# Performance work log

Hardware: AMD Instinct MI355X
Metric: run time of the kernel (lower is better)

## Reference

```python
import jax, jax.numpy as jnp
import numpy as np

B = 32768   # batch of states (original forward is per-state; we vmap)
D = 3       # coord_dim

_W_SHAPES = [("w_h0",(3,32)),("w_y0",(3,32)),("w_yu0",(3,3)),("w_u0",(3,32)),
             ("w_h1",(32,32)),("w_z1",(32,32)),("w_zu1",(32,32)),("w_y1",(3,32)),
             ("w_yu1",(32,3)),("w_u1",(32,32)),("w_h2",(32,32)),("w_z2",(32,32)),
             ("w_zu2",(32,32)),("w_y2",(3,32)),("w_yu2",(32,3)),("w_u2",(32,32)),
             ("w_z_out",(32,1)),("w_zu_out",(32,32)),("w_y_out",(3,1)),
             ("w_yu_out",(32,3)),("w_u_out",(32,1))]
_B_SHAPES = [("b_y0",(3,)),("b_h0",(32,)),("b_0",(32,)),("b_h1",(32,)),("b_y1",(3,)),
             ("b_z1",(32,)),("b_1",(32,)),("b_h2",(32,)),("b_z2",(32,)),("b_y2",(3,)),
             ("b_2",(32,)),("b_z_out",(32,)),("b_y_out",(3,)),("b_out",(1,))]

def _make_params(key):
    n = len(_W_SHAPES) + len(_B_SHAPES) + 4
    ks = jax.random.split(key, n)
    p, i = {}, 0
    for name, sh in _W_SHAPES:   # torch .uniform_(-0.1, 0.1)
        p[name] = jax.random.uniform(ks[i], sh, jnp.float32, -0.1, 0.1); i += 1
    for name, sh in _B_SHAPES:   # torch.rand -> U[0,1)
        p[name] = jax.random.uniform(ks[i], sh, jnp.float32, 0.0, 1.0); i += 1
    # fc layers: normal init per _init_weights (stds / sqrt(16)=4), zero bias
    stds = [2.2/4.0, 0.58/4.0, 0.58*2.0/4.0, 4.0]
    shapes = [(32, 3), (32, 32), (32, 32), (1, 32)]
    for j in range(4):
        p[f"fc{j+1}_w"] = stds[j] * jax.random.normal(ks[i], shapes[j], jnp.float32); i += 1
        p[f"fc{j+1}_b"] = jnp.zeros((shapes[j][0],), jnp.float32)
    return p

def setup_inputs():
    key = jax.random.key(0)
    kx, kp = jax.random.split(key)
    inp = {"x": jax.random.normal(kx, (B, 2 * D), jnp.float32)}
    inp.update(_make_params(kp))
    return inp

def _forward(x, p):
    sp, relu = jax.nn.softplus, jax.nn.relu

    def lagr(state):
        q, y = state[:D], state[D:]
        u1 = sp(q @ p["w_h0"] + p["b_h0"])
        z1 = sp((y * (q @ p["w_yu0"] + p["b_y0"])) @ p["w_y0"] + q @ p["w_u0"] + p["b_0"])
        u2 = sp(u1 @ p["w_h1"] + p["b_h1"])
        z2 = sp((z1 * (u1 @ p["w_zu1"] + p["b_z1"])) @ relu(p["w_z1"])
                + (y * (u1 @ p["w_yu1"] + p["b_y1"])) @ p["w_y1"]
                + u1 @ p["w_u1"] + p["b_1"])
        u3 = sp(u2 @ p["w_h2"] + p["b_h2"])
        z3 = sp((z2 * (u2 @ p["w_zu2"] + p["b_z2"])) @ relu(p["w_z2"])
                + (y * (u2 @ p["w_yu2"] + p["b_y2"])) @ p["w_y2"]
                + u2 @ p["w_u2"] + p["b_2"])
        zout = sp((z3 * (u3 @ p["w_zu_out"] + p["b_z_out"])) @ relu(p["w_z_out"])
                  + (y * (u3 @ p["w_yu_out"] + p["b_y_out"])) @ p["w_y_out"]
                  + u3 @ p["w_u_out"] + p["b_out"])
        V = sp(q @ p["fc1_w"].T + p["fc1_b"])
        V = sp(V @ p["fc2_w"].T + p["fc2_b"])
        V = sp(V @ p["fc3_w"].T + p["fc3_b"])
        V = V @ p["fc4_w"].T + p["fc4_b"]
        return (zout - V)[0]  # scalar Lagrangian

    def step(state):
        dq = state[D:]
        H = jax.hessian(lagr)(state)        # (6,6)
        g = jax.grad(lagr)(state)[:D]       # dL/dq, matches jacobian row b[0,:3]
        M = H[D:, D:]                       # d2L/ddq ddq
        C = H[D:, :D]                       # d2L/ddq dq
        ddq = (g - dq @ C.T) @ jnp.linalg.inv(M).T
        dx = jnp.concatenate([dq, ddq])
        return state + 0.001 * dx           # Euler step, as in torch forward

    return jax.vmap(step)(x)

def reference(x, w_h0, w_y0, w_yu0, w_u0, w_h1, w_z1, w_zu1, w_y1, w_yu1, w_u1,
              w_h2, w_z2, w_zu2, w_y2, w_yu2, w_u2, w_z_out, w_zu_out, w_y_out,
              w_yu_out, w_u_out, b_y0, b_h0, b_0, b_h1, b_y1, b_z1, b_1, b_h2,
              b_z2, b_y2, b_2, b_z_out, b_y_out, b_out, fc1_w, fc1_b, fc2_w,
              fc2_b, fc3_w, fc3_b, fc4_w, fc4_b):
    p = dict(locals())
    xv = p.pop("x")
    return _forward(xv, p)
```

## Files before the change

kernel.cpp:

```cpp
#include <hip/hip_runtime.h>

#define NTH 256
#define B_TOTAL 32768

typedef float v2f __attribute__((ext_vector_type(2)));
typedef float v4f __attribute__((ext_vector_type(4)));

struct Ptrs { const float* p[44]; };

enum : int {
  I_X = 0,
  I_WH0 = 1, I_WY0 = 2, I_WYU0 = 3, I_WU0 = 4,
  I_WH1 = 5, I_WZ1 = 6, I_WZU1 = 7, I_WY1 = 8, I_WYU1 = 9, I_WU1 = 10,
  I_WH2 = 11, I_WZ2 = 12, I_WZU2 = 13, I_WY2 = 14, I_WYU2 = 15, I_WU2 = 16,
  I_WZO = 17, I_WZUO = 18, I_WYO = 19, I_WYUO = 20, I_WUO = 21,
  I_BY0 = 22, I_BH0 = 23, I_B0 = 24, I_BH1 = 25, I_BY1 = 26, I_BZ1 = 27, I_B1 = 28,
  I_BH2 = 29, I_BZ2 = 30, I_BY2 = 31, I_B2 = 32, I_BZO = 33, I_BYO = 34, I_BOUT = 35,
  I_FC1 = 36, I_FC1B = 37, I_FC2 = 38, I_FC2B = 39, I_FC3 = 40, I_FC3B = 41,
  I_FC4 = 42, I_FC4B = 43
};

struct V16 { float c[16]; };

__device__ __forceinline__ float spf(float x) {
  return fmaxf(x, 0.0f) + __logf(1.0f + __expf(-fabsf(x)));
}
__device__ __forceinline__ float sigf(float x) {
  return __fdividef(1.0f, 1.0f + __expf(-x));
}

__device__ __forceinline__ V16 spchain16(const V16& A, float y0, float y1, float y2) {
  V16 Z;
  float s = sigf(A.c[0]);
  float d = s * (1.0f - s);
  Z.c[0] = spf(A.c[0]);
#pragma unroll
  for (int a = 0; a < 3; ++a) Z.c[1 + a] = s * A.c[1 + a];
#pragma unroll
  for (int b = 0; b < 3; ++b) Z.c[4 + b] = s * A.c[4 + b];
  Z.c[7]  = s * A.c[7]  + d * A.c[1] * A.c[1];
  Z.c[8]  = s * A.c[8]  + d * A.c[1] * A.c[2];
  Z.c[9]  = s * A.c[9]  + d * A.c[1] * A.c[3];
  Z.c[10] = s * A.c[10] + d * A.c[2] * A.c[2];
  Z.c[11] = s * A.c[11] + d * A.c[2] * A.c[3];
  Z.c[12] = s * A.c[12] + d * A.c[3] * A.c[3];
  float ydq = y0 * A.c[4] + y1 * A.c[5] + y2 * A.c[6];
#pragma unroll
  for (int a = 0; a < 3; ++a) Z.c[13 + a] = s * A.c[13 + a] + d * A.c[1 + a] * ydq;
  return Z;
}

__device__ __forceinline__ void stageProd(float* row, const V16& Z, float S0, float S1,
                                          float S2, float S3, float y0, float y1, float y2) {
  float z0 = Z.c[0];
  float ysd = y0 * S1 + y1 * S2 + y2 * S3;
  v4f w0 = {z0 * S0, S0 * Z.c[1], S0 * Z.c[2], S0 * Z.c[3]};
  v4f w1 = {z0 * S1 + S0 * Z.c[4], z0 * S2 + S0 * Z.c[5], z0 * S3 + S0 * Z.c[6], S0 * Z.c[7]};
  v4f w2 = {S0 * Z.c[8], S0 * Z.c[9], S0 * Z.c[10], S0 * Z.c[11]};
  v4f w3 = {S0 * Z.c[12], S0 * Z.c[13] + Z.c[1] * ysd, S0 * Z.c[14] + Z.c[2] * ysd,
            S0 * Z.c[15] + Z.c[3] * ysd};
  *(v4f*)(row + 0) = w0;  *(v4f*)(row + 4) = w1;
  *(v4f*)(row + 8) = w2;  *(v4f*)(row + 12) = w3;
}

__device__ __forceinline__ V16 prodZS16(const V16& Z, float S0, float S1, float S2, float S3,
                                        float y0, float y1, float y2) {
  V16 P;
  const float Sq[3] = {S1, S2, S3};
  float ysd = y0 * S1 + y1 * S2 + y2 * S3;
  P.c[0] = Z.c[0] * S0;
#pragma unroll
  for (int a = 0; a < 3; ++a) P.c[1 + a] = S0 * Z.c[1 + a];
#pragma unroll
  for (int b = 0; b < 3; ++b) P.c[4 + b] = Z.c[0] * Sq[b] + S0 * Z.c[4 + b];
#pragma unroll
  for (int t = 0; t < 6; ++t) P.c[7 + t] = S0 * Z.c[7 + t];
#pragma unroll
  for (int a = 0; a < 3; ++a) P.c[13 + a] = S0 * Z.c[13 + a] + Z.c[1 + a] * ysd;
  return P;
}

__device__ __forceinline__ void mv16(const float* __restrict__ W, int j, const float* ps,
                                     v2f& m0, v2f& m1, v2f& m2, v2f& m3,
                                     v2f& m4, v2f& m5, v2f& m6, v2f& m7) {
#pragma unroll 4
  for (int i = 0; i < 32; ++i) {
    float w = fmaxf(W[i * 32 + j], 0.0f);
    const float* r = ps + i * 16;
    v4f r0 = *(const v4f*)(r + 0);
    v4f r1 = *(const v4f*)(r + 4);
    v4f r2 = *(const v4f*)(r + 8);
    v4f r3 = *(const v4f*)(r + 12);
    m0 += r0.xy * w; m1 += r0.zw * w;
    m2 += r1.xy * w; m3 += r1.zw * w;
    m4 += r2.xy * w; m5 += r2.zw * w;
    m6 += r3.xy * w; m7 += r3.zw * w;
  }
}

__device__ __forceinline__ void stageU_all(const float* __restrict__ Wh,
                                           const float* __restrict__ Wzu,
                                           const float* __restrict__ Wu,
                                           const float* __restrict__ Wyu, int j,
                                           const float* us,
                                           v2f& h0, v2f& h1, v2f& s0, v2f& s1,
                                           v2f& w0, v2f& w1,
                                           v2f& ta0, v2f& ta1, v2f& tb0, v2f& tb1,
                                           v2f& tc0, v2f& tc1) {
#pragma unroll 2
  for (int i = 0; i < 32; ++i) {
    v4f u = *(const v4f*)(us + i * 4);
    float wh = Wh[i * 32 + j], wz = Wzu[i * 32 + j], wu = Wu[i * 32 + j];
    h0 += u.xy * wh; h1 += u.zw * wh;
    s0 += u.xy * wz; s1 += u.zw * wz;
    w0 += u.xy * wu; w1 += u.zw * wu;
    float wy0 = Wyu[i * 3 + 0], wy1 = Wyu[i * 3 + 1], wy2 = Wyu[i * 3 + 2];
    ta0 += u.xy * wy0; ta1 += u.zw * wy0;
    tb0 += u.xy * wy1; tb1 += u.zw * wy1;
    tc0 += u.xy * wy2; tc1 += u.zw * wy2;
  }
}

__device__ __forceinline__ void buildA16(const float* __restrict__ Wy, int j, float y0, float y1,
                                         float y2, const float wv[4], const float ta[4],
                                         const float tb[4], const float tc[4], V16& A) {
  float wy0 = Wy[j], wy1 = Wy[32 + j], wy2 = Wy[64 + j];
  A.c[0] = wv[0] + y0 * ta[0] * wy0 + y1 * tb[0] * wy1 + y2 * tc[0] * wy2;
  A.c[1] = ta[0] * wy0; A.c[2] = tb[0] * wy1; A.c[3] = tc[0] * wy2;
#pragma unroll
  for (int b = 0; b < 3; ++b)
    A.c[4 + b] = wv[1 + b] + y0 * ta[1 + b] * wy0 + y1 * tb[1 + b] * wy1 + y2 * tc[1 + b] * wy2;
#pragma unroll
  for (int t6 = 0; t6 < 6; ++t6) A.c[7 + t6] = 0.0f;
  float yta = y0 * ta[1] + y1 * ta[2] + y2 * ta[3];
  float ytb = y0 * tb[1] + y1 * tb[2] + y2 * tb[3];
  float ytc = y0 * tc[1] + y1 * tc[2] + y2 * tc[3];
  A.c[13] = yta * wy0; A.c[14] = ytb * wy1; A.c[15] = ytc * wy2;
}

__global__ __launch_bounds__(NTH, 4) void lnn_step_kernel(Ptrs P, float* __restrict__ out) {
  __shared__ float pstage[4][2][32][16];
  __shared__ float ustage[4][2][32][4];

  const int tid = threadIdx.x;
  const int j = tid & 31;
  const int half = (tid >> 5) & 1;
  const int wv = tid >> 6;
  const int sample = blockIdx.x * 8 + (tid >> 5);

  float* prow = &pstage[wv][half][0][0];
  float* urow = &ustage[wv][half][0][0];

  const float* X = P.p[I_X] + sample * 6;
  const float q0 = X[0], q1 = X[1], q2 = X[2];
  const float y0 = X[3], y1 = X[4], y2 = X[5];

  float Vg0, Vg1, Vg2;
  {
    const float* fc1 = P.p[I_FC1];
    float f0 = fc1[j * 3], f1 = fc1[j * 3 + 1], f2 = fc1[j * 3 + 2];
    float hp = P.p[I_FC1B][j] + q0 * f0 + q1 * f1 + q2 * f2;
    float ss = sigf(hp);
    v4f V1 = {spf(hp), ss * f0, ss * f1, ss * f2};
    *(v4f*)(urow + j * 4) = V1;
    const float* fc2 = P.p[I_FC2] + j * 32;
    v2f a0 = {P.p[I_FC2B][j], 0.0f}, a1 = {0.0f, 0.0f};
#pragma unroll 2
    for (int r = 0; r < 8; ++r) {
      v4f w4 = *(const v4f*)(fc2 + r * 4);
      v4f u0 = *(const v4f*)(urow + (r * 4 + 0) * 4);
      v4f u1 = *(const v4f*)(urow + (r * 4 + 1) * 4);
      v4f u2 = *(const v4f*)(urow + (r * 4 + 2) * 4);
      v4f u3 = *(const v4f*)(urow + (r * 4 + 3) * 4);
      a0 += u0.xy * w4.x; a1 += u0.zw * w4.x;
      a0 += u1.xy * w4.y; a1 += u1.zw * w4.y;
      a0 += u2.xy * w4.z; a1 += u2.zw * w4.z;
      a0 += u3.xy * w4.w; a1 += u3.zw * w4.w;
    }
    float ss2 = sigf(a0.x);
    v4f V2 = {spf(a0.x), ss2 * a0.y, ss2 * a1.x, ss2 * a1.y};
    *(v4f*)(urow + j * 4) = V2;
    const float* fc3 = P.p[I_FC3] + j * 32;
    v2f b0 = {P.p[I_FC3B][j], 0.0f}, b1 = {0.0f, 0.0f};
#pragma unroll 2
    for (int r = 0; r < 8; ++r) {
      v4f w4 = *(const v4f*)(fc3 + r * 4);
      v4f u0 = *(const v4f*)(urow + (r * 4 + 0) * 4);
      v4f u1 = *(const v4f*)(urow + (r * 4 + 1) * 4);
      v4f u2 = *(const v4f*)(urow + (r * 4 + 2) * 4);
      v4f u3 = *(const v4f*)(urow + (r * 4 + 3) * 4);
      b0 += u0.xy * w4.x; b1 += u0.zw * w4.x;
      b0 += u1.xy * w4.y; b1 += u1.zw * w4.y;
      b0 += u2.xy * w4.z; b1 += u2.zw * w4.z;
      b0 += u3.xy * w4.w; b1 += u3.zw * w4.w;
    }
    float ss3 = sigf(b0.x);
    float f4 = P.p[I_FC4][j];
    Vg0 = ss3 * b0.y * f4; Vg1 = ss3 * b1.x * f4; Vg2 = ss3 * b1.y * f4;
  }

  const float* yu0 = P.p[I_WYU0];
  float t0v[3];
#pragma unroll
  for (int k = 0; k < 3; ++k)
    t0v[k] = q0 * yu0[k] + q1 * yu0[3 + k] + q2 * yu0[6 + k] + P.p[I_BY0][k];

  float u1c[4];
  {
    const float* wh0 = P.p[I_WH0];
    float w0 = wh0[j], w1 = wh0[32 + j], w2 = wh0[64 + j];
    float h = P.p[I_BH0][j] + q0 * w0 + q1 * w1 + q2 * w2;
    float ss = sigf(h);
    u1c[0] = spf(h); u1c[1] = ss * w0; u1c[2] = ss * w1; u1c[3] = ss * w2;
  }

  V16 z;
  {
    const float* Wy = P.p[I_WY0];
    const float* Wu = P.p[I_WU0];
    float wy0 = Wy[j], wy1 = Wy[32 + j], wy2 = Wy[64 + j];
    float wu0 = Wu[j], wu1 = Wu[32 + j], wu2 = Wu[64 + j];
    V16 A;
    A.c[0] = P.p[I_B0][j] + (y0 * t0v[0]) * wy0 + (y1 * t0v[1]) * wy1 + (y2 * t0v[2]) * wy2 +
             q0 * wu0 + q1 * wu1 + q2 * wu2;
    A.c[1] = t0v[0] * wy0; A.c[2] = t0v[1] * wy1; A.c[3] = t0v[2] * wy2;
#pragma unroll
    for (int b = 0; b < 3; ++b) {
      float acc = (b == 0 ? wu0 : (b == 1 ? wu1 : wu2));
      acc += y0 * yu0[b * 3 + 0] * wy0 + y1 * yu0[b * 3 + 1] * wy1 + y2 * yu0[b * 3 + 2] * wy2;
      A.c[4 + b] = acc;
    }
#pragma unroll
    for (int t = 0; t < 6; ++t) A.c[7 + t] = 0.0f;
    float yty0 = y0 * yu0[0] + y1 * yu0[3] + y2 * yu0[6];
    float yty1 = y0 * yu0[1] + y1 * yu0[4] + y2 * yu0[7];
    float yty2 = y0 * yu0[2] + y1 * yu0[5] + y2 * yu0[8];
    A.c[13] = yty0 * wy0; A.c[14] = yty1 * wy1; A.c[15] = yty2 * wy2;
    z = spchain16(A, y0, y1, y2);
  }

  float unext[4];
#pragma unroll 1
  for (int lvl = 0; lvl < 2; ++lvl) {
    const float* Wh  = P.p[lvl == 0 ? I_WH1 : I_WH2];
    const float* Wzu = P.p[lvl == 0 ? I_WZU1 : I_WZU2];
    const float* Wu  = P.p[lvl == 0 ? I_WU1 : I_WU2];
    const float* Wyu = P.p[lvl == 0 ? I_WYU1 : I_WYU2];
    const float* Wy  = P.p[lvl == 0 ? I_WY1 : I_WY2];
    const float* Wz  = P.p[lvl == 0 ? I_WZ1 : I_WZ2];
    const float* Bh  = P.p[lvl == 0 ? I_BH1 : I_BH2];
    const float* Bz  = P.p[lvl == 0 ? I_BZ1 : I_BZ2];
    const float* Bl  = P.p[lvl == 0 ? I_B1 : I_B2];
    const float* By  = P.p[lvl == 0 ? I_BY1 : I_BY2];

    const float* uc = (lvl == 0) ? u1c : unext;
    v4f uu = {uc[0], uc[1], uc[2], uc[3]};
    *(v4f*)(urow + j * 4) = uu;

    v2f h0 = {Bh[j], 0.0f}, h1 = {0.0f, 0.0f};
    v2f s0 = {Bz[j], 0.0f}, s1 = {0.0f, 0.0f};
    v2f w0 = {Bl[j], 0.0f}, w1 = {0.0f, 0.0f};
    v2f ta0 = {By[0], 0.0f}, ta1 = {0.0f, 0.0f};
    v2f tb0 = {By[1], 0.0f}, tb1 = {0.0f, 0.0f};
    v2f tc0 = {By[2], 0.0f}, tc1 = {0.0f, 0.0f};
    stageU_all(Wh, Wzu, Wu, Wyu, j, urow, h0, h1, s0, s1, w0, w1,
               ta0, ta1, tb0, tb1, tc0, tc1);
    {
      float ss = sigf(h0.x);
      unext[0] = spf(h0.x); unext[1] = ss * h0.y; unext[2] = ss * h1.x; unext[3] = ss * h1.y;
    }
    stageProd(prow + j * 16, z, s0.x, s0.y, s1.x, s1.y, y0, y1, y2);

    float wvv[4] = {w0.x, w0.y, w1.x, w1.y};
    float tav[4] = {ta0.x, ta0.y, ta1.x, ta1.y};
    float tbv[4] = {tb0.x, tb0.y, tb1.x, tb1.y};
    float tcv[4] = {tc0.x, tc0.y, tc1.x, tc1.y};
    V16 A2;
    buildA16(Wy, j, y0, y1, y2, wvv, tav, tbv, tcv, A2);

    v2f m0 = {A2.c[0], A2.c[1]},   m1 = {A2.c[2], A2.c[3]};
    v2f m2 = {A2.c[4], A2.c[5]},   m3 = {A2.c[6], A2.c[7]};
    v2f m4 = {A2.c[8], A2.c[9]},   m5 = {A2.c[10], A2.c[11]};
    v2f m6 = {A2.c[12], A2.c[13]}, m7 = {A2.c[14], A2.c[15]};
    mv16(Wz, j, prow, m0, m1, m2, m3, m4, m5, m6, m7);
    A2.c[0] = m0.x;  A2.c[1] = m0.y;  A2.c[2] = m1.x;  A2.c[3] = m1.y;
    A2.c[4] = m2.x;  A2.c[5] = m2.y;  A2.c[6] = m3.x;  A2.c[7] = m3.y;
    A2.c[8] = m4.x;  A2.c[9] = m4.y;  A2.c[10] = m5.x; A2.c[11] = m5.y;
    A2.c[12] = m6.x; A2.c[13] = m6.y; A2.c[14] = m7.x; A2.c[15] = m7.y;
    z = spchain16(A2, y0, y1, y2);
  }

  {
    v4f uu = {unext[0], unext[1], unext[2], unext[3]};
    *(v4f*)(urow + j * 4) = uu;
  }
  v2f s30 = {P.p[I_BZO][j], 0.0f}, s31 = {0.0f, 0.0f};
  v2f wo0 = {0.0f, 0.0f}, wo1 = {0.0f, 0.0f};
  v2f t3a0 = {P.p[I_BYO][0], 0.0f}, t3a1 = {0.0f, 0.0f};
  v2f t3b0 = {P.p[I_BYO][1], 0.0f}, t3b1 = {0.0f, 0.0f};
  v2f t3c0 = {P.p[I_BYO][2], 0.0f}, t3c1 = {0.0f, 0.0f};
  {
    const float* Wzuo = P.p[I_WZUO];
    const float* Wuo = P.p[I_WUO];
    const float* Wyuo = P.p[I_WYUO];
#pragma unroll 2
    for (int i = 0; i < 32; ++i) {
      v4f u = *(const v4f*)(urow + i * 4);
      float wz = Wzuo[i * 32 + j];
      s30 += u.xy * wz; s31 += u.zw * wz;
      float wu = Wuo[i];
      wo0 += u.xy * wu; wo1 += u.zw * wu;
      float wy0 = Wyuo[i * 3], wy1 = Wyuo[i * 3 + 1], wy2 = Wyuo[i * 3 + 2];
      t3a0 += u.xy * wy0; t3a1 += u.zw * wy0;
      t3b0 += u.xy * wy1; t3b1 += u.zw * wy1;
      t3c0 += u.xy * wy2; t3c1 += u.zw * wy2;
    }
  }
  const float woc[4] = {wo0.x, wo0.y, wo1.x, wo1.y};
  const float t3av[4] = {t3a0.x, t3a0.y, t3a1.x, t3a1.y};
  const float t3bv[4] = {t3b0.x, t3b0.y, t3b1.x, t3b1.y};
  const float t3cv[4] = {t3c0.x, t3c0.y, t3c1.x, t3c1.y};

  float red[19];
  {
    V16 p3 = prodZS16(z, s30.x, s30.y, s31.x, s31.y, y0, y1, y2);
    float wz = fmaxf(P.p[I_WZO][j], 0.0f);
#pragma unroll
    for (int k = 0; k < 16; ++k) red[k] = p3.c[k] * wz;
    red[16] = Vg0; red[17] = Vg1; red[18] = Vg2;
  }
#pragma unroll
  for (int m = 16; m >= 1; m >>= 1) {
#pragma unroll
    for (int k = 0; k < 19; ++k) red[k] += __shfl_xor(red[k], m, 32);
  }

  if (j == 0) {
    const float* Wyo = P.p[I_WYO];
    const float wyo0 = Wyo[0], wyo1 = Wyo[1], wyo2 = Wyo[2];
    float Av = red[0] + woc[0] + P.p[I_BOUT][0] + y0 * t3av[0] * wyo0 +
               y1 * t3bv[0] * wyo1 + y2 * t3cv[0] * wyo2;
    float Agy[3];
    Agy[0] = red[1] + t3av[0] * wyo0;
    Agy[1] = red[2] + t3bv[0] * wyo1;
    Agy[2] = red[3] + t3cv[0] * wyo2;
    float Agq[3];
#pragma unroll
    for (int b = 0; b < 3; ++b)
      Agq[b] = red[4 + b] + woc[1 + b] + y0 * t3av[1 + b] * wyo0 +
               y1 * t3bv[1 + b] * wyo1 + y2 * t3cv[1 + b] * wyo2;
    float ycq[3];
    ycq[0] = red[13] + (y0 * t3av[1] + y1 * t3av[2] + y2 * t3av[3]) * wyo0;
    ycq[1] = red[14] + (y0 * t3bv[1] + y1 * t3bv[2] + y2 * t3bv[3]) * wyo1;
    ycq[2] = red[15] + (y0 * t3cv[1] + y1 * t3cv[2] + y2 * t3cv[3]) * wyo2;
    float s = sigf(Av), d = s * (1.0f - s);

    double Mm[3][3];
    const int pa[6] = {0, 0, 0, 1, 1, 2}, pb[6] = {0, 1, 2, 1, 2, 2};
#pragma unroll
    for (int t = 0; t < 6; ++t) {
      double m = (double)s * (double)red[7 + t] +
                 (double)d * (double)Agy[pa[t]] * (double)Agy[pb[t]];
      Mm[pa[t]][pb[t]] = m; Mm[pb[t]][pa[t]] = m;
    }
    double yAgq = (double)y0 * (double)Agq[0] + (double)y1 * (double)Agq[1] +
                  (double)y2 * (double)Agq[2];
    double rr[3];
#pragma unroll
    for (int a = 0; a < 3; ++a) {
      double g = (double)s * (double)Agq[a] - (double)red[16 + a];
      double Cy = (double)s * (double)ycq[a] + (double)d * (double)Agy[a] * yAgq;
      rr[a] = g - Cy;
    }
    double a = Mm[0][0], b_ = Mm[0][1], c_ = Mm[0][2], dd = Mm[1][1], e = Mm[1][2], f = Mm[2][2];
    double A00 = dd * f - e * e, A01 = c_ * e - b_ * f, A02 = b_ * e - c_ * dd;
    double A11 = a * f - c_ * c_, A12 = b_ * c_ - a * e, A22 = a * dd - b_ * b_;
    double det = a * A00 + b_ * A01 + c_ * A02;
    double idet = 1.0 / det;
    double d0 = (A00 * rr[0] + A01 * rr[1] + A02 * rr[2]) * idet;
    double d1 = (A01 * rr[0] + A11 * rr[1] + A12 * rr[2]) * idet;
    double d2 = (A02 * rr[0] + A12 * rr[1] + A22 * rr[2]) * idet;

    float* O = out + (size_t)sample * 6;
    O[0] = q0 + 0.001f * y0;
    O[1] = q1 + 0.001f * y1;
    O[2] = q2 + 0.001f * y2;
    O[3] = y0 + 0.001f * (float)d0;
    O[4] = y1 + 0.001f * (float)d1;
    O[5] = y2 + 0.001f * (float)d2;
  }
}

extern "C" void kernel_launch(void* const* d_in, const int* in_sizes, int n_in,
                              void* d_out, int out_size, void* d_ws, size_t ws_size,
                              hipStream_t stream) {
  (void)in_sizes; (void)n_in; (void)d_ws; (void)ws_size; (void)out_size;
  Ptrs P;
  for (int i = 0; i < 44; ++i) P.p[i] = (const float*)d_in[i];
  float* out = (float*)d_out;
  dim3 grid(B_TOTAL / 8), block(NTH);
  hipLaunchKernelGGL(lnn_step_kernel, grid, block, 0, stream, P, out);
}
```

Before: 135.2 us.

## Replace scalar relu(Wz) matvec with FP64 MFMA over staged shared-memory tiles

The per-lane 32x16 scalar matvec against relu(W_z) in the hidden-level loop is replaced by a wave-level 32x32 by 32x16 matrix product using FP64 16x16x4 MFMA instructions over both half-wave sample tiles. Each lane stages its product row into shared memory, the wave multiplies collectively, and results go back to shared memory to be added into the tangent accumulators. The shared-memory row stride is padded from 16 to 20 floats to reduce bank conflicts. The FP64 MFMA rate and the float-double conversions may limit the gain, and the cross-lane shared-memory traffic has no explicit barrier beyond wave-level lockstep.

```diff
diff --git a/kernel.cpp b/kernel.cpp
--- a/kernel.cpp
+++ b/kernel.cpp
@@ -2,9 +2,11 @@
 
 #define NTH 256
 #define B_TOTAL 32768
+#define PSTR 20
 
 typedef float v2f __attribute__((ext_vector_type(2)));
 typedef float v4f __attribute__((ext_vector_type(4)));
+typedef double v4d __attribute__((ext_vector_type(4)));
 
 struct Ptrs { const float* p[44]; };
 
@@ -78,24 +80,6 @@
 #pragma unroll
   for (int a = 0; a < 3; ++a) P.c[13 + a] = S0 * Z.c[13 + a] + Z.c[1 + a] * ysd;
   return P;
-}
-
-__device__ __forceinline__ void mv16(const float* __restrict__ W, int j, const float* ps,
-                                     v2f& m0, v2f& m1, v2f& m2, v2f& m3,
-                                     v2f& m4, v2f& m5, v2f& m6, v2f& m7) {
-#pragma unroll 4
-  for (int i = 0; i < 32; ++i) {
-    float w = fmaxf(W[i * 32 + j], 0.0f);
-    const float* r = ps + i * 16;
-    v4f r0 = *(const v4f*)(r + 0);
-    v4f r1 = *(const v4f*)(r + 4);
-    v4f r2 = *(const v4f*)(r + 8);
-    v4f r3 = *(const v4f*)(r + 12);
-    m0 += r0.xy * w; m1 += r0.zw * w;
-    m2 += r1.xy * w; m3 += r1.zw * w;
-    m4 += r2.xy * w; m5 += r2.zw * w;
-    m6 += r3.xy * w; m7 += r3.zw * w;
-  }
 }
 
 __device__ __forceinline__ void stageU_all(const float* __restrict__ Wh,
@@ -139,7 +123,7 @@
 }
 
 __global__ __launch_bounds__(NTH, 4) void lnn_step_kernel(Ptrs P, float* __restrict__ out) {
-  __shared__ float pstage[4][2][32][16];
+  __shared__ float pstage[4][2][32][PSTR];
   __shared__ float ustage[4][2][32][4];
 
   const int tid = threadIdx.x;
@@ -150,6 +134,11 @@
 
   float* prow = &pstage[wv][half][0][0];
   float* urow = &ustage[wv][half][0][0];
+  float* pst0 = &pstage[wv][0][0][0];
+  float* pst1 = &pstage[wv][1][0][0];
+  const int l64 = tid & 63;
+  const int n16 = l64 & 15;
+  const int kq = l64 >> 4;
 
   const float* X = P.p[I_X] + sample * 6;
   const float q0 = X[0], q1 = X[1], q2 = X[2];
@@ -269,7 +258,31 @@
       float ss = sigf(h0.x);
       unext[0] = spf(h0.x); unext[1] = ss * h0.y; unext[2] = ss * h1.x; unext[3] = ss * h1.y;
     }
-    stageProd(prow + j * 16, z, s0.x, s0.y, s1.x, s1.y, y0, y1, y2);
+    stageProd(prow + j * PSTR, z, s0.x, s0.y, s1.x, s1.y, y0, y1, y2);
+
+    v4d a00 = {0.0, 0.0, 0.0, 0.0};
+    v4d a01 = {0.0, 0.0, 0.0, 0.0};
+    v4d a10 = {0.0, 0.0, 0.0, 0.0};
+    v4d a11 = {0.0, 0.0, 0.0, 0.0};
+#pragma unroll
+    for (int c = 0; c < 8; ++c) {
+      const int i = c * 4 + kq;
+      double b0 = (double)pst0[i * PSTR + n16];
+      double b1 = (double)pst1[i * PSTR + n16];
+      double wlo = (double)fmaxf(Wz[i * 32 + n16], 0.0f);
+      double whi = (double)fmaxf(Wz[i * 32 + 16 + n16], 0.0f);
+      a00 = __builtin_amdgcn_mfma_f64_16x16x4f64(wlo, b0, a00, 0, 0, 0);
+      a01 = __builtin_amdgcn_mfma_f64_16x16x4f64(whi, b0, a01, 0, 0, 0);
+      a10 = __builtin_amdgcn_mfma_f64_16x16x4f64(wlo, b1, a10, 0, 0, 0);
+      a11 = __builtin_amdgcn_mfma_f64_16x16x4f64(whi, b1, a11, 0, 0, 0);
+    }
+#pragma unroll
+    for (int r = 0; r < 4; ++r) {
+      pst0[(kq + 4 * r) * PSTR + n16]        = (float)a00[r];
+      pst0[(16 + kq + 4 * r) * PSTR + n16]   = (float)a01[r];
+      pst1[(kq + 4 * r) * PSTR + n16]        = (float)a10[r];
+      pst1[(16 + kq + 4 * r) * PSTR + n16]   = (float)a11[r];
+    }
 
     float wvv[4] = {w0.x, w0.y, w1.x, w1.y};
     float tav[4] = {ta0.x, ta0.y, ta1.x, ta1.y};
@@ -278,15 +291,17 @@
     V16 A2;
     buildA16(Wy, j, y0, y1, y2, wvv, tav, tbv, tcv, A2);
 
-    v2f m0 = {A2.c[0], A2.c[1]},   m1 = {A2.c[2], A2.c[3]};
-    v2f m2 = {A2.c[4], A2.c[5]},   m3 = {A2.c[6], A2.c[7]};
-    v2f m4 = {A2.c[8], A2.c[9]},   m5 = {A2.c[10], A2.c[11]};
-    v2f m6 = {A2.c[12], A2.c[13]}, m7 = {A2.c[14], A2.c[15]};
-    mv16(Wz, j, prow, m0, m1, m2, m3, m4, m5, m6, m7);
-    A2.c[0] = m0.x;  A2.c[1] = m0.y;  A2.c[2] = m1.x;  A2.c[3] = m1.y;
-    A2.c[4] = m2.x;  A2.c[5] = m2.y;  A2.c[6] = m3.x;  A2.c[7] = m3.y;
-    A2.c[8] = m4.x;  A2.c[9] = m4.y;  A2.c[10] = m5.x; A2.c[11] = m5.y;
-    A2.c[12] = m6.x; A2.c[13] = m6.y; A2.c[14] = m7.x; A2.c[15] = m7.y;
+    {
+      const float* rown = prow + j * PSTR;
+      v4f r0 = *(const v4f*)(rown + 0);
+      v4f r1 = *(const v4f*)(rown + 4);
+      v4f r2 = *(const v4f*)(rown + 8);
+      v4f r3 = *(const v4f*)(rown + 12);
+      A2.c[0] += r0.x;  A2.c[1] += r0.y;  A2.c[2] += r0.z;  A2.c[3] += r0.w;
+      A2.c[4] += r1.x;  A2.c[5] += r1.y;  A2.c[6] += r1.z;  A2.c[7] += r1.w;
+      A2.c[8] += r2.x;  A2.c[9] += r2.y;  A2.c[10] += r2.z; A2.c[11] += r2.w;
+      A2.c[12] += r3.x; A2.c[13] += r3.y; A2.c[14] += r3.z; A2.c[15] += r3.w;
+    }
     z = spchain16(A2, y0, y1, y2);
   }
 
```

New measurement: 131.5 us. 1.03x faster.
